# Kernel tuning notes

Hardware: AMD Instinct MI355X
Metric: run time of the kernel (lower is better)

## Reference

```python
import jax, jax.numpy as jnp
import numpy as np

LN_EPS = 1e-7

def gelu(x):
    # BERT erf-based gelu
    return 0.5 * x * (1.0 + jax.lax.erf(x / jnp.sqrt(2.0).astype(x.dtype)))

def setup_inputs() -> dict:
    key = jax.random.key(0)
    k1, k2 = jax.random.split(key)
    B, S, H, I = 4, 4096, 1024, 4096
    hidden_states = jax.random.normal(k1, (B, S, H), dtype=jnp.float32)
    W = jax.random.normal(k2, (H, I), dtype=jnp.float32) * (1.0 / np.sqrt(H))
    b = jnp.zeros((I,), dtype=jnp.float32)
    ln_gamma = jnp.ones((H,), dtype=jnp.float32)
    ln_beta = jnp.zeros((H,), dtype=jnp.float32)
    return {"hidden_states": hidden_states, "ln_gamma": ln_gamma, "ln_beta": ln_beta, "W": W, "b": b}

def reference(hidden_states, ln_gamma, ln_beta, W, b):
    # LayerNorm over last dim
    mu = jnp.mean(hidden_states, axis=-1, keepdims=True)
    xc = hidden_states - mu
    var = jnp.mean(xc * xc, axis=-1, keepdims=True)
    x_norm = xc * jax.lax.rsqrt(var + LN_EPS) * ln_gamma + ln_beta
    # Linear projection [B,S,H] @ [H,I] + b, then gelu
    y = jnp.einsum('bsh,hi->bsi', x_norm, W) + b
    return gelu(y)
```

## Files before the change

### kernel.cpp

```cpp
#include <hip/hip_runtime.h>
#include <hip/hip_bf16.h>

typedef __attribute__((ext_vector_type(8))) short bf16x8;
typedef __attribute__((ext_vector_type(4))) float f32x4;

static __device__ __forceinline__ unsigned short f2bf(float f) {
    unsigned u = __builtin_bit_cast(unsigned, f);
    unsigned rounding = 0x7fffu + ((u >> 16) & 1u);
    u += rounding;
    return (unsigned short)(u >> 16);
}

static __device__ __forceinline__ void async_copy16(const void* g, void* l) {
    __builtin_amdgcn_global_load_lds(
        (const __attribute__((address_space(1))) unsigned int*)g,
        (__attribute__((address_space(3))) unsigned int*)l,
        16, 0, 0);
}

#define BARRIER() __builtin_amdgcn_s_barrier()
#define VMCNT(N) do { asm volatile("s_waitcnt vmcnt(" #N ")" ::: "memory"); \
                      __builtin_amdgcn_sched_barrier(0); } while (0)
#define VM0() VMCNT(0)

static __device__ __forceinline__ float fast_gelu(float y) {
    float u = 0.7978845608028654f * y * (1.0f + 0.044715f * y * y);
    float au = fminf(fabsf(u), 9.0f);
    float e = __expf(-2.0f * au);
    float th = (1.0f - e) * __builtin_amdgcn_rcpf(1.0f + e);
    th = (u < 0.0f) ? -th : th;
    return 0.5f * y * (1.0f + th);
}

__global__ __launch_bounds__(256) void prep_kernel(
    const float* __restrict__ x, const float* __restrict__ gamma,
    const float* __restrict__ beta, unsigned short* __restrict__ Aout,
    const float* __restrict__ W, unsigned short* __restrict__ Wt) {
    __shared__ float smem[33 * 32];
    const int b = blockIdx.x;
    const int t = threadIdx.x;

    if (b < 16384) {
        const int row = b;
        const float4 v = ((const float4*)(x + (size_t)row * 1024))[t];
        float s  = v.x + v.y + v.z + v.w;
        float ss = v.x * v.x + v.y * v.y + v.z * v.z + v.w * v.w;
        #pragma unroll
        for (int off = 32; off; off >>= 1) {
            s  += __shfl_down(s, off);
            ss += __shfl_down(ss, off);
        }
        const int wid = t >> 6, lane = t & 63;
        if (lane == 0) { smem[wid] = s; smem[wid + 4] = ss; }
        __syncthreads();
        if (t == 0) {
            float S  = smem[0] + smem[1] + smem[2] + smem[3];
            float SS = smem[4] + smem[5] + smem[6] + smem[7];
            float mu = S * (1.0f / 1024.0f);
            float var = SS * (1.0f / 1024.0f) - mu * mu;
            smem[0] = mu;
            smem[1] = rsqrtf(var + 1e-7f);
        }
        __syncthreads();
        const float mu = smem[0], rs = smem[1];
        const float4 g = ((const float4*)gamma)[t];
        const float4 be = ((const float4*)beta)[t];
        ushort4 pk;
        pk.x = f2bf((v.x - mu) * rs * g.x + be.x);
        pk.y = f2bf((v.y - mu) * rs * g.y + be.y);
        pk.z = f2bf((v.z - mu) * rs * g.z + be.z);
        pk.w = f2bf((v.w - mu) * rs * g.w + be.w);
        ((ushort4*)(Aout + (size_t)row * 1024))[t] = pk;
    } else {
        const int r = b - 16384;
        const int bx = r & 127;
        const int by = r >> 7;
        float (*tile)[33] = (float(*)[33])smem;
        const int tx = t & 31;
        const int ty = t >> 5;
        #pragma unroll
        for (int i = 0; i < 4; ++i) {
            int k = by * 32 + ty + i * 8;
            tile[ty + i * 8][tx] = W[(size_t)k * 4096 + bx * 32 + tx];
        }
        __syncthreads();
        #pragma unroll
        for (int i = 0; i < 4; ++i) {
            int n = bx * 32 + ty + i * 8;
            Wt[(size_t)n * 1024 + by * 32 + tx] = f2bf(tile[tx][ty + i * 8]);
        }
    }
}

__global__ __launch_bounds__(512, 1) void gemm_kernel(
    const unsigned short* __restrict__ A, const unsigned short* __restrict__ Wt,
    const float* __restrict__ bias, float* __restrict__ out) {
    __shared__ char lds_mem[131072];

    const int bid = blockIdx.x;
    const int t = threadIdx.x;
    const int lane = t & 63;
    const int wid = t >> 6;
    const int wm = wid >> 2;
    const int wn = wid & 3;
    const int lrow = lane & 15;
    const int lk = lane >> 4;

    const int srr = t >> 3;
    const int sch = t & 7;
    const int sgc = sch ^ (srr & 7);
    const int lst = srr * 128 + sch * 16;

    const int ck0 = ((lk) ^ (lrow & 7)) * 16;
    const int ck1 = ((4 + lk) ^ (lrow & 7)) * 16;
    const int aBase = (wm * 128 + lrow) * 128;
    const int bBase = 32768 + (wn * 64 + lrow) * 128;

    char* lds0 = lds_mem;
    char* lds1 = lds_mem + 65536;

    const unsigned short *gA, *gB;
    int bm, bn;
    auto tileBase = [&](int tau) {
        const int swz = (tau & 7) * 128 + (tau >> 3);
        bm = swz >> 4;
        bn = swz & 15;
        gA = A  + (size_t)(bm * 256 + srr) * 1024 + sgc * 8;
        gB = Wt + (size_t)(bn * 256 + srr) * 1024 + sgc * 8;
    };

    auto stageB = [&](const unsigned short* pB, int kt, char* buf) {
        #pragma unroll
        for (int i = 0; i < 4; ++i)
            async_copy16(pB + (size_t)(i * 64) * 1024 + kt * 64,
                         buf + 32768 + i * 8192 + lst);
    };
    auto stageA = [&](const unsigned short* pA, int kt, char* buf) {
        async_copy16(pA + kt * 64,                      buf + lst);
        async_copy16(pA + (size_t)131072 + kt * 64,     buf + 16384 + lst);
        async_copy16(pA + (size_t)65536  + kt * 64,     buf + 8192  + lst);
        async_copy16(pA + (size_t)196608 + kt * 64,     buf + 24576 + lst);
    };

    tileBase(bid);
    stageB(gB, 0, lds0);
    stageA(gA, 0, lds0);
    VM0();
    BARRIER();

    const int NKT = 16;
    for (int i = 0; i < 4; ++i) {
        const int bmc = bm, bnc = bn;
        float bv[4];
        #pragma unroll
        for (int ni = 0; ni < 4; ++ni) bv[ni] = bias[bnc * 256 + wn * 64 + ni * 16 + lrow];

        f32x4 acc[8][4];
        #pragma unroll
        for (int a = 0; a < 8; ++a)
            #pragma unroll
            for (int j = 0; j < 4; ++j) acc[a][j] = (f32x4)0.0f;

        for (int kt = 0; kt < NKT; ++kt) {
            char* cbuf = (kt & 1) ? lds1 : lds0;
            char* nbuf = (kt & 1) ? lds0 : lds1;
            const bool haveNext = (kt < NKT - 1) || (i < 3);
            if (kt == NKT - 1 && i < 3) tileBase(bid + 256 * (i + 1));
            const int ktn = (kt < NKT - 1) ? kt + 1 : 0;

            bf16x8 bf[4][2];
            #pragma unroll
            for (int ni = 0; ni < 4; ++ni) {
                const char* p = cbuf + bBase + ni * 16 * 128;
                bf[ni][0] = *(const bf16x8*)(p + ck0);
                bf[ni][1] = *(const bf16x8*)(p + ck1);
            }
            bf16x8 af[4][2];
            #pragma unroll
            for (int mi = 0; mi < 4; ++mi) {
                const char* p = cbuf + aBase + mi * 16 * 128;
                af[mi][0] = *(const bf16x8*)(p + ck0);
                af[mi][1] = *(const bf16x8*)(p + ck1);
            }
            if (haveNext) stageB(gB, ktn, nbuf);
            __builtin_amdgcn_s_setprio(1);
            #pragma unroll
            for (int mi = 0; mi < 4; ++mi)
                #pragma unroll
                for (int ni = 0; ni < 4; ++ni) {
                    acc[mi][ni] = __builtin_amdgcn_mfma_f32_16x16x32_bf16(af[mi][0], bf[ni][0], acc[mi][ni], 0, 0, 0);
                    acc[mi][ni] = __builtin_amdgcn_mfma_f32_16x16x32_bf16(af[mi][1], bf[ni][1], acc[mi][ni], 0, 0, 0);
                }
            __builtin_amdgcn_s_setprio(0);
            if (!haveNext) {
                VM0();
            } else if (kt > 0) {
                VMCNT(4);
            }
            BARRIER();

            bf16x8 ag[4][2];
            #pragma unroll
            for (int mi = 0; mi < 4; ++mi) {
                const char* p = cbuf + aBase + (64 + mi * 16) * 128;
                ag[mi][0] = *(const bf16x8*)(p + ck0);
                ag[mi][1] = *(const bf16x8*)(p + ck1);
            }
            if (haveNext) stageA(gA, ktn, nbuf);
            __builtin_amdgcn_s_setprio(1);
            #pragma unroll
            for (int mi = 0; mi < 4; ++mi)
                #pragma unroll
                for (int ni = 0; ni < 4; ++ni) {
                    acc[4 + mi][ni] = __builtin_amdgcn_mfma_f32_16x16x32_bf16(ag[mi][0], bf[ni][0], acc[4 + mi][ni], 0, 0, 0);
                    acc[4 + mi][ni] = __builtin_amdgcn_mfma_f32_16x16x32_bf16(ag[mi][1], bf[ni][1], acc[4 + mi][ni], 0, 0, 0);
                }
            __builtin_amdgcn_s_setprio(0);
            if (kt == NKT - 1) {
                VM0();
            } else {
                VMCNT(2);
            }
            BARRIER();
        }

        #pragma unroll
        for (int mi = 0; mi < 8; ++mi) {
            const int row0 = bmc * 256 + wm * 128 + mi * 16 + lk * 4;
            #pragma unroll
            for (int ni = 0; ni < 4; ++ni) {
                const int col = bnc * 256 + wn * 64 + ni * 16 + lrow;
                #pragma unroll
                for (int r = 0; r < 4; ++r) {
                    float y = acc[mi][ni][r] + bv[ni];
                    out[(size_t)(row0 + r) * 4096 + col] = fast_gelu(y);
                }
            }
        }
    }
}

extern "C" void kernel_launch(void* const* d_in, const int* in_sizes, int n_in,
                              void* d_out, int out_size, void* d_ws, size_t ws_size,
                              hipStream_t stream) {
    const float* hidden = (const float*)d_in[0];
    const float* gamma  = (const float*)d_in[1];
    const float* beta   = (const float*)d_in[2];
    const float* W      = (const float*)d_in[3];
    const float* bias   = (const float*)d_in[4];
    float* out = (float*)d_out;

    unsigned short* Abf = (unsigned short*)d_ws;
    unsigned short* Wt  = (unsigned short*)((char*)d_ws + (size_t)16384 * 1024 * 2);

    prep_kernel<<<16384 + 4096, 256, 0, stream>>>(hidden, gamma, beta, Abf, W, Wt);
    gemm_kernel<<<256, 512, 0, stream>>>(Abf, Wt, bias, out);
}
```

Baseline: 177.9 us.

## Replace persistent GEMM with one-tile-per-block grid and four-phase split pipeline

Switches from 256 persistent blocks, each looping over 4 output tiles, to 1024 blocks that each compute a single 256x256 tile. The inner k-loop becomes a four-phase schedule: A and B halves are staged in separate quarter-loads, interleaved with quadrant MFMA groups under more barriers and explicit lgkmcnt waits. The aim is finer-grained overlap of global-to-LDS copies with MFMA work, and removal of the cross-tile prefetch logic. The cost is extra barriers per k-step and a pipeline prologue and epilogue paid for every tile instead of being amortized across four.

```diff
diff --git a/kernel.cpp b/kernel.cpp
--- a/kernel.cpp
+++ b/kernel.cpp
@@ -22,6 +22,8 @@
 #define VMCNT(N) do { asm volatile("s_waitcnt vmcnt(" #N ")" ::: "memory"); \
                       __builtin_amdgcn_sched_barrier(0); } while (0)
 #define VM0() VMCNT(0)
+#define LGKM0()  do { asm volatile("s_waitcnt lgkmcnt(0)" ::: "memory"); \
+                      __builtin_amdgcn_sched_barrier(0); } while (0)
 
 static __device__ __forceinline__ float fast_gelu(float y) {
     float u = 0.7978845608028654f * y * (1.0f + 0.044715f * y * y);
@@ -98,6 +100,10 @@
     __shared__ char lds_mem[131072];
 
     const int bid = blockIdx.x;
+    const int swz = (bid & 7) * 128 + (bid >> 3);
+    const int bm = swz >> 4;
+    const int bn = swz & 15;
+
     const int t = threadIdx.x;
     const int lane = t & 63;
     const int wid = t >> 6;
@@ -106,10 +112,41 @@
     const int lrow = lane & 15;
     const int lk = lane >> 4;
 
-    const int srr = t >> 3;
+    const int sra = t >> 3;
+    const int srb = ((t >> 3) & 31) + (((t >> 3) >> 5) << 6);
     const int sch = t & 7;
-    const int sgc = sch ^ (srr & 7);
-    const int lst = srr * 128 + sch * 16;
+    const int sgc = sch ^ (sra & 7);
+    const unsigned short* gAb = A  + (size_t)(bm * 256) * 1024 + sgc * 8;
+    const unsigned short* gBb = Wt + (size_t)(bn * 256) * 1024 + sgc * 8;
+
+    auto stAm0 = [&](int kt, char* buf) {
+        #pragma unroll
+        for (int j = 0; j < 2; ++j) {
+            const int row = j * 128 + sra;
+            async_copy16(gAb + (size_t)row * 1024 + kt * 64, buf + row * 128 + sch * 16);
+        }
+    };
+    auto stAm1 = [&](int kt, char* buf) {
+        #pragma unroll
+        for (int j = 0; j < 2; ++j) {
+            const int row = j * 128 + 64 + sra;
+            async_copy16(gAb + (size_t)row * 1024 + kt * 64, buf + row * 128 + sch * 16);
+        }
+    };
+    auto stBn0 = [&](int kt, char* buf) {
+        #pragma unroll
+        for (int j = 0; j < 2; ++j) {
+            const int row = j * 128 + srb;
+            async_copy16(gBb + (size_t)row * 1024 + kt * 64, buf + 32768 + row * 128 + sch * 16);
+        }
+    };
+    auto stBn1 = [&](int kt, char* buf) {
+        #pragma unroll
+        for (int j = 0; j < 2; ++j) {
+            const int row = j * 128 + 32 + srb;
+            async_copy16(gBb + (size_t)row * 1024 + kt * 64, buf + 32768 + row * 128 + sch * 16);
+        }
+    };
 
     const int ck0 = ((lk) ^ (lrow & 7)) * 16;
     const int ck1 = ((4 + lk) ^ (lrow & 7)) * 16;
@@ -119,122 +156,124 @@
     char* lds0 = lds_mem;
     char* lds1 = lds_mem + 65536;
 
-    const unsigned short *gA, *gB;
-    int bm, bn;
-    auto tileBase = [&](int tau) {
-        const int swz = (tau & 7) * 128 + (tau >> 3);
-        bm = swz >> 4;
-        bn = swz & 15;
-        gA = A  + (size_t)(bm * 256 + srr) * 1024 + sgc * 8;
-        gB = Wt + (size_t)(bn * 256 + srr) * 1024 + sgc * 8;
-    };
-
-    auto stageB = [&](const unsigned short* pB, int kt, char* buf) {
-        #pragma unroll
-        for (int i = 0; i < 4; ++i)
-            async_copy16(pB + (size_t)(i * 64) * 1024 + kt * 64,
-                         buf + 32768 + i * 8192 + lst);
-    };
-    auto stageA = [&](const unsigned short* pA, int kt, char* buf) {
-        async_copy16(pA + kt * 64,                      buf + lst);
-        async_copy16(pA + (size_t)131072 + kt * 64,     buf + 16384 + lst);
-        async_copy16(pA + (size_t)65536  + kt * 64,     buf + 8192  + lst);
-        async_copy16(pA + (size_t)196608 + kt * 64,     buf + 24576 + lst);
-    };
-
-    tileBase(bid);
-    stageB(gB, 0, lds0);
-    stageA(gA, 0, lds0);
+    f32x4 acc[8][4];
+    #pragma unroll
+    for (int a = 0; a < 8; ++a)
+        #pragma unroll
+        for (int j = 0; j < 4; ++j) acc[a][j] = (f32x4)0.0f;
+
+    float bv[4];
+    #pragma unroll
+    for (int j = 0; j < 4; ++j) bv[j] = bias[bn * 256 + wn * 64 + j * 16 + lrow];
+
+    stAm0(0, lds0); stBn0(0, lds0); stBn1(0, lds0); stAm1(0, lds0);
     VM0();
     BARRIER();
 
     const int NKT = 16;
-    for (int i = 0; i < 4; ++i) {
-        const int bmc = bm, bnc = bn;
-        float bv[4];
-        #pragma unroll
-        for (int ni = 0; ni < 4; ++ni) bv[ni] = bias[bnc * 256 + wn * 64 + ni * 16 + lrow];
-
-        f32x4 acc[8][4];
-        #pragma unroll
-        for (int a = 0; a < 8; ++a)
-            #pragma unroll
-            for (int j = 0; j < 4; ++j) acc[a][j] = (f32x4)0.0f;
-
-        for (int kt = 0; kt < NKT; ++kt) {
-            char* cbuf = (kt & 1) ? lds1 : lds0;
-            char* nbuf = (kt & 1) ? lds0 : lds1;
-            const bool haveNext = (kt < NKT - 1) || (i < 3);
-            if (kt == NKT - 1 && i < 3) tileBase(bid + 256 * (i + 1));
-            const int ktn = (kt < NKT - 1) ? kt + 1 : 0;
-
-            bf16x8 bf[4][2];
-            #pragma unroll
-            for (int ni = 0; ni < 4; ++ni) {
-                const char* p = cbuf + bBase + ni * 16 * 128;
-                bf[ni][0] = *(const bf16x8*)(p + ck0);
-                bf[ni][1] = *(const bf16x8*)(p + ck1);
-            }
-            bf16x8 af[4][2];
-            #pragma unroll
-            for (int mi = 0; mi < 4; ++mi) {
-                const char* p = cbuf + aBase + mi * 16 * 128;
-                af[mi][0] = *(const bf16x8*)(p + ck0);
-                af[mi][1] = *(const bf16x8*)(p + ck1);
-            }
-            if (haveNext) stageB(gB, ktn, nbuf);
-            __builtin_amdgcn_s_setprio(1);
-            #pragma unroll
-            for (int mi = 0; mi < 4; ++mi)
-                #pragma unroll
-                for (int ni = 0; ni < 4; ++ni) {
-                    acc[mi][ni] = __builtin_amdgcn_mfma_f32_16x16x32_bf16(af[mi][0], bf[ni][0], acc[mi][ni], 0, 0, 0);
-                    acc[mi][ni] = __builtin_amdgcn_mfma_f32_16x16x32_bf16(af[mi][1], bf[ni][1], acc[mi][ni], 0, 0, 0);
-                }
-            __builtin_amdgcn_s_setprio(0);
-            if (!haveNext) {
-                VM0();
-            } else if (kt > 0) {
-                VMCNT(4);
-            }
+    for (int kt = 0; kt < NKT; ++kt) {
+        char* cbuf = (kt & 1) ? lds1 : lds0;
+        char* nbuf = (kt & 1) ? lds0 : lds1;
+        const bool hn = (kt + 1 < NKT);
+        const int ktn = kt + 1;
+
+        bf16x8 af[4][2], bf0[2][2], bf1[2][2];
+
+        #pragma unroll
+        for (int mi = 0; mi < 4; ++mi) {
+            const char* p = cbuf + aBase + mi * 16 * 128;
+            af[mi][0] = *(const bf16x8*)(p + ck0);
+            af[mi][1] = *(const bf16x8*)(p + ck1);
+        }
+        #pragma unroll
+        for (int ni = 0; ni < 2; ++ni) {
+            const char* p = cbuf + bBase + ni * 16 * 128;
+            bf0[ni][0] = *(const bf16x8*)(p + ck0);
+            bf0[ni][1] = *(const bf16x8*)(p + ck1);
+        }
+        if (hn) stAm0(ktn, nbuf);
+        BARRIER();
+        LGKM0();
+        __builtin_amdgcn_s_setprio(1);
+        #pragma unroll
+        for (int mi = 0; mi < 4; ++mi)
+            #pragma unroll
+            for (int ni = 0; ni < 2; ++ni) {
+                acc[mi][ni] = __builtin_amdgcn_mfma_f32_16x16x32_bf16(af[mi][0], bf0[ni][0], acc[mi][ni], 0, 0, 0);
+                acc[mi][ni] = __builtin_amdgcn_mfma_f32_16x16x32_bf16(af[mi][1], bf0[ni][1], acc[mi][ni], 0, 0, 0);
+            }
+        __builtin_amdgcn_s_setprio(0);
+        if (hn) { VMCNT(4); } else { VMCNT(2); }
+        BARRIER();
+
+        #pragma unroll
+        for (int ni = 0; ni < 2; ++ni) {
+            const char* p = cbuf + bBase + (32 + ni * 16) * 128;
+            bf1[ni][0] = *(const bf16x8*)(p + ck0);
+            bf1[ni][1] = *(const bf16x8*)(p + ck1);
+        }
+        if (hn) stBn0(ktn, nbuf);
+        BARRIER();
+        LGKM0();
+        __builtin_amdgcn_s_setprio(1);
+        #pragma unroll
+        for (int mi = 0; mi < 4; ++mi)
+            #pragma unroll
+            for (int ni = 0; ni < 2; ++ni) {
+                acc[mi][2 + ni] = __builtin_amdgcn_mfma_f32_16x16x32_bf16(af[mi][0], bf1[ni][0], acc[mi][2 + ni], 0, 0, 0);
+                acc[mi][2 + ni] = __builtin_amdgcn_mfma_f32_16x16x32_bf16(af[mi][1], bf1[ni][1], acc[mi][2 + ni], 0, 0, 0);
+            }
+        __builtin_amdgcn_s_setprio(0);
+        if (hn) { VMCNT(4); } else { VM0(); }
+        BARRIER();
+
+        #pragma unroll
+        for (int mi = 0; mi < 4; ++mi) {
+            const char* p = cbuf + aBase + (64 + mi * 16) * 128;
+            af[mi][0] = *(const bf16x8*)(p + ck0);
+            af[mi][1] = *(const bf16x8*)(p + ck1);
+        }
+        if (hn) stBn1(ktn, nbuf);
+        BARRIER();
+        LGKM0();
+        __builtin_amdgcn_s_setprio(1);
+        #pragma unroll
+        for (int mi = 0; mi < 4; ++mi)
+            #pragma unroll
+            for (int ni = 0; ni < 2; ++ni) {
+                acc[4 + mi][2 + ni] = __builtin_amdgcn_mfma_f32_16x16x32_bf16(af[mi][0], bf1[ni][0], acc[4 + mi][2 + ni], 0, 0, 0);
+                acc[4 + mi][2 + ni] = __builtin_amdgcn_mfma_f32_16x16x32_bf16(af[mi][1], bf1[ni][1], acc[4 + mi][2 + ni], 0, 0, 0);
+            }
+        __builtin_amdgcn_s_setprio(0);
+        BARRIER();
+
+        if (hn) stAm1(ktn, nbuf);
+        BARRIER();
+        __builtin_amdgcn_s_setprio(1);
+        #pragma unroll
+        for (int mi = 0; mi < 4; ++mi)
+            #pragma unroll
+            for (int ni = 0; ni < 2; ++ni) {
+                acc[4 + mi][ni] = __builtin_amdgcn_mfma_f32_16x16x32_bf16(af[mi][0], bf0[ni][0], acc[4 + mi][ni], 0, 0, 0);
+                acc[4 + mi][ni] = __builtin_amdgcn_mfma_f32_16x16x32_bf16(af[mi][1], bf0[ni][1], acc[4 + mi][ni], 0, 0, 0);
+            }
+        __builtin_amdgcn_s_setprio(0);
+        if (hn) {
+            VMCNT(4);
             BARRIER();
-
-            bf16x8 ag[4][2];
-            #pragma unroll
-            for (int mi = 0; mi < 4; ++mi) {
-                const char* p = cbuf + aBase + (64 + mi * 16) * 128;
-                ag[mi][0] = *(const bf16x8*)(p + ck0);
-                ag[mi][1] = *(const bf16x8*)(p + ck1);
-            }
-            if (haveNext) stageA(gA, ktn, nbuf);
-            __builtin_amdgcn_s_setprio(1);
-            #pragma unroll
-            for (int mi = 0; mi < 4; ++mi)
-                #pragma unroll
-                for (int ni = 0; ni < 4; ++ni) {
-                    acc[4 + mi][ni] = __builtin_amdgcn_mfma_f32_16x16x32_bf16(ag[mi][0], bf[ni][0], acc[4 + mi][ni], 0, 0, 0);
-                    acc[4 + mi][ni] = __builtin_amdgcn_mfma_f32_16x16x32_bf16(ag[mi][1], bf[ni][1], acc[4 + mi][ni], 0, 0, 0);
-                }
-            __builtin_amdgcn_s_setprio(0);
-            if (kt == NKT - 1) {
-                VM0();
-            } else {
-                VMCNT(2);
-            }
-            BARRIER();
-        }
-
-        #pragma unroll
-        for (int mi = 0; mi < 8; ++mi) {
-            const int row0 = bmc * 256 + wm * 128 + mi * 16 + lk * 4;
-            #pragma unroll
-            for (int ni = 0; ni < 4; ++ni) {
-                const int col = bnc * 256 + wn * 64 + ni * 16 + lrow;
-                #pragma unroll
-                for (int r = 0; r < 4; ++r) {
-                    float y = acc[mi][ni][r] + bv[ni];
-                    out[(size_t)(row0 + r) * 4096 + col] = fast_gelu(y);
-                }
+        }
+    }
+
+    #pragma unroll
+    for (int mi = 0; mi < 8; ++mi) {
+        const int row0 = bm * 256 + wm * 128 + mi * 16 + lk * 4;
+        #pragma unroll
+        for (int j = 0; j < 4; ++j) {
+            const int col = bn * 256 + wn * 64 + j * 16 + lrow;
+            #pragma unroll
+            for (int r = 0; r < 4; ++r) {
+                float y = acc[mi][j][r] + bv[j];
+                out[(size_t)(row0 + r) * 4096 + col] = fast_gelu(y);
             }
         }
     }
@@ -254,5 +293,5 @@
     unsigned short* Wt  = (unsigned short*)((char*)d_ws + (size_t)16384 * 1024 * 2);
 
     prep_kernel<<<16384 + 4096, 256, 0, stream>>>(hidden, gamma, beta, Abf, W, Wt);
-    gemm_kernel<<<256, 512, 0, stream>>>(Abf, Wt, bias, out);
-}
+    gemm_kernel<<<1024, 512, 0, stream>>>(Abf, Wt, bias, out);
+}
```

Result: slower. 184.9 us (+3.9%).
